# Kernel optimization log

Hardware: AMD Instinct MI355X
Metric: run time of the kernel (lower is better)

Reference implementation:

```python
import jax, jax.numpy as jnp
import numpy as np

GAMMA = 0.96875
ROPE_THETA = 10000.0


def _rope(x):
    # x: (B, S, d) -> rotary applied over interleaved pairs (torchtune-style)
    B, S, d = x.shape
    inv_freq = 1.0 / (ROPE_THETA ** (jnp.arange(0, d, 2, dtype=jnp.float32) / d))  # (d/2,)
    angles = jnp.arange(S, dtype=jnp.float32)[:, None] * inv_freq[None, :]  # (S, d/2)
    cos = jnp.cos(angles).astype(x.dtype)
    sin = jnp.sin(angles).astype(x.dtype)
    xs = x.reshape(B, S, d // 2, 2)
    x0, x1 = xs[..., 0], xs[..., 1]
    out = jnp.stack([x0 * cos - x1 * sin, x1 * cos + x0 * sin], axis=-1)
    return out.reshape(B, S, d)


def _decay_mask(S, dtype):
    n = jnp.arange(S)[:, None]
    m = jnp.arange(S)[None, :]
    diff = n - m
    # gamma^(n-m) for n>=m else 0; clamp exponent to avoid inf/nan
    D = jnp.exp(jnp.maximum(diff, 0).astype(jnp.float32) * np.log(GAMMA))
    return jnp.where(diff >= 0, D, 0.0).astype(dtype)


def setup_inputs() -> dict:
    key = jax.random.key(0)
    k1, k2, k3, k4 = jax.random.split(key, 4)
    H = 256
    X = jax.random.normal(k1, (4, 8192, H), dtype=jnp.float32)
    W_Q = jax.random.normal(k2, (H, H), dtype=jnp.float32) / H
    W_K = jax.random.normal(k3, (H, H), dtype=jnp.float32) / H
    W_V = jax.random.normal(k4, (H, H), dtype=jnp.float32) / H
    return {"X": X, "W_Q": W_Q, "W_K": W_K, "W_V": W_V}


def reference(X, W_Q, W_K, W_V):
    B, S, _ = X.shape
    D = _decay_mask(S, X.dtype)  # (S, S)
    Q = _rope(X @ W_Q)  # (B, S, d)
    K = _rope(X @ W_K)
    V = X @ W_V  # (B, S, v_dim)
    ret = jnp.einsum('bqd,bkd->bqk', Q, K) * D[None]  # (B, S, S)
    return ret @ V
```

## Files before the change

### kernel.cpp

```cpp
#include <hip/hip_runtime.h>
#include <hip/hip_bf16.h>

#define B_  4
#define S_  8192
#define H_  256
#define C_  128
#define NC_ 64
#define M_  (B_*S_)

typedef unsigned short u16;
typedef __attribute__((ext_vector_type(8))) short short8;
typedef __attribute__((ext_vector_type(4))) float f32x4;
typedef __attribute__((address_space(1))) void gas_t;
typedef __attribute__((address_space(3))) void las_t;

static constexpr float L2G   = -0.045803690f;
static constexpr float ROPE2 = -0.103810253f;

__device__ __forceinline__ u16 f2b(float x) {
  union { __hip_bfloat16 b; u16 u; } c; c.b = __float2bfloat16(x); return c.u;
}
__device__ __forceinline__ float b2f(u16 u) {
  union { u16 u; __hip_bfloat16 b; } c; c.u = u; return __bfloat162float(c.b);
}
__device__ __forceinline__ f32x4 mfma16(short8 a, short8 b, f32x4 c) {
  return __builtin_amdgcn_mfma_f32_16x16x32_bf16(a, b, c, 0, 0, 0);
}

__device__ __forceinline__ int sw4(int row) { return (row ^ (row >> 2)) & 3; }
__device__ __forceinline__ short8 fr32(const u16* base, int row, int slot) {
  return *reinterpret_cast<const short8*>(base + row*256 + (((slot&24)|((slot&7)^(row&7)))<<3));
}
__device__ __forceinline__ short8 fr16(const u16* base, int row, int slot) {
  return *reinterpret_cast<const short8*>(base + row*128 + (((slot&8)|((slot&7)^(row&7)))<<3));
}
__device__ __forceinline__ short8 fr4(const u16* base, int row, int slot) {
  return *reinterpret_cast<const short8*>(base + row*32 + ((slot ^ sw4(row))<<3));
}
__device__ __forceinline__ short8 fragr(const u16* lds, int row, int slot) {
  return *reinterpret_cast<const short8*>(lds + row*64 + ((slot ^ (row & 7)) << 3));
}

__device__ __forceinline__ void stageA(const u16* __restrict__ src, int stride,
                                       u16* smbase, int off, int t) {
  #pragma unroll
  for (int it = 0; it < 4; ++it) {
    const int u = it*256 + t, row = u >> 3, lsl = (u & 7) ^ (row & 7);
    const u16* gp = src + (size_t)row*stride + lsl*8;
    u16* lp = smbase + off + it*2048 + (t & 192)*8;
    __builtin_amdgcn_global_load_lds((gas_t*)gp, (las_t*)lp, 16, 0, 0);
  }
}
__device__ __forceinline__ void stageW(const u16* __restrict__ src, u16* dst, int t) {
  #pragma unroll
  for (int it = 0; it < 2; ++it) {
    const int u = it*512 + t, row = u >> 2, p = u & 3, s = p ^ sw4(row);
    const u16* gp = src + (size_t)row*256 + s*8;
    u16* lp = dst + (size_t)(it*512 + (t & ~63))*8;
    __builtin_amdgcn_global_load_lds((gas_t*)gp, (las_t*)lp, 16, 0, 0);
  }
}

__global__ __launch_bounds__(256) void prep(
    const float* __restrict__ Wq, const float* __restrict__ Wk,
    const float* __restrict__ Wv, u16* __restrict__ WhT, float* __restrict__ RTab)
{
  const int bid = blockIdx.x;
  if (bid < 96) {
    const int i = bid*256 + threadIdx.x;
    const int z = i >> 13, r = i & 8191;
    const int n = r >> 5, k0 = (r & 31) << 3;
    const float* W = (z == 0) ? Wq : (z == 1) ? Wk : Wv;
    u16 o[8];
    #pragma unroll
    for (int j = 0; j < 8; ++j) o[j] = f2b(W[(size_t)(k0 + j)*H_ + n]);
    *reinterpret_cast<uint4*>(WhT + ((size_t)z << 16) + n*H_ + k0) =
        *reinterpret_cast<uint4*>(o);
    return;
  }
  const int i = (bid - 96)*256 + threadIdx.x;
  const int s = i >> 7, h = i & 127;
  const float invf = exp2f(ROPE2 * (float)h);
  float sn, cs;
  sincosf((float)s * invf, &sn, &cs);
  *reinterpret_cast<float2*>(RTab + 2*((size_t)s*128 + h)) = make_float2(cs, sn);
}

__global__ __launch_bounds__(512, 2) void fused_chunk(
    const float* __restrict__ X, const u16* __restrict__ WhT,
    const float* __restrict__ RTab,
    u16* __restrict__ Qh, u16* __restrict__ Tt,
    u16* __restrict__ Scg, u16* __restrict__ VTg)
{
  __shared__ u16 SM[81920];
  u16* XS = SM;
  u16* WB = SM + 32768;
  u16* RB = SM + 49152;
  const int t = threadIdx.x, l = t & 63, wid = t >> 6;
  const int g = l >> 4, l15 = l & 15;
  const int mr = wid >> 2, nq = wid & 3;
  const int c = blockIdx.x, b = blockIdx.y;
  const float* Xc = X + ((size_t)(b*S_ + c*C_))*H_;
  const float4* RT4 = reinterpret_cast<const float4*>(RTab);

  stageW(WhT + 0, WB, t);
  #pragma unroll
  for (int it = 0; it < 8; ++it) {
    const int u = it*512 + t, row = u >> 5, sl = u & 31;
    const float* p = Xc + (size_t)row*256 + sl*8;
    float4 a = *reinterpret_cast<const float4*>(p);
    float4 bb = *reinterpret_cast<const float4*>(p + 4);
    u16 o[8] = {f2b(a.x), f2b(a.y), f2b(a.z), f2b(a.w),
                f2b(bb.x), f2b(bb.y), f2b(bb.z), f2b(bb.w)};
    *reinterpret_cast<uint4*>(XS + row*256 + (((sl&24)|((sl&7)^(row&7)))<<3)) =
        *reinterpret_cast<uint4*>(o);
  }
  __syncthreads();

  f32x4 qa[4][4] = {};
  for (int ks = 0; ks < 8; ++ks) {
    const u16* Wcur = WB + (ks&1)*8192;
    if (ks < 7) stageW(WhT + (ks+1)*32, WB + ((ks+1)&1)*8192, t);
    short8 a[4], bw[4];
    #pragma unroll
    for (int i = 0; i < 4; ++i) a[i] = fr32(XS, mr*64 + i*16 + l15, ks*4 + g);
    #pragma unroll
    for (int j = 0; j < 4; ++j) bw[j] = fr4(Wcur, nq*64 + j*16 + l15, g);
    #pragma unroll
    for (int i = 0; i < 4; ++i)
      #pragma unroll
      for (int j = 0; j < 4; ++j)
        qa[i][j] = mfma16(bw[j], a[i], qa[i][j]);
    __syncthreads();
  }
  #pragma unroll
  for (int i = 0; i < 4; ++i) {
    const int s = c*C_ + mr*64 + i*16 + l15;
    #pragma unroll
    for (int j = 0; j < 4; ++j) {
      const int n0 = nq*64 + j*16 + g*4;
      const float4 tb = RT4[(size_t)s*64 + (n0 >> 2)];
      const float x0 = qa[i][j][0], x1 = qa[i][j][1];
      const float x2 = qa[i][j][2], x3 = qa[i][j][3];
      qa[i][j][0] = x0*tb.x - x1*tb.y;  qa[i][j][1] = x1*tb.x + x0*tb.y;
      qa[i][j][2] = x2*tb.z - x3*tb.w;  qa[i][j][3] = x3*tb.z + x2*tb.w;
    }
  }
  #pragma unroll
  for (int i = 0; i < 4; ++i) {
    const int m = mr*64 + i*16 + l15;
    #pragma unroll
    for (int j = 0; j < 4; ++j) {
      const int n0 = nq*64 + j*16 + g*4;
      ushort4 pk;
      pk.x = f2b(qa[i][j][0]); pk.y = f2b(qa[i][j][1]);
      pk.z = f2b(qa[i][j][2]); pk.w = f2b(qa[i][j][3]);
      const int sl = n0 >> 3;
      *reinterpret_cast<ushort4*>(RB + m*256 + (((sl&24)|((sl&7)^(m&7)))<<3) + (n0&7)) = pk;
    }
  }
  __syncthreads();
  #pragma unroll
  for (int it = 0; it < 8; ++it) {
    const int u = it*512 + t, row = u >> 5, sl = u & 31;
    uint4 v = *reinterpret_cast<const uint4*>(RB + row*256 + (((sl&24)|((sl&7)^(row&7)))<<3));
    *reinterpret_cast<uint4*>(Qh + ((size_t)(b*S_ + c*C_ + row))*H_ + sl*8) = v;
  }

  f32x4 ka[4][4] = {};
  stageW(WhT + 65536, WB, t);
  __syncthreads();
  for (int ks = 0; ks < 8; ++ks) {
    const u16* Wcur = WB + (ks&1)*8192;
    if (ks < 7) stageW(WhT + 65536 + (ks+1)*32, WB + ((ks+1)&1)*8192, t);
    short8 a[4], bw[4];
    #pragma unroll
    for (int i = 0; i < 4; ++i) a[i] = fr32(XS, mr*64 + i*16 + l15, ks*4 + g);
    #pragma unroll
    for (int j = 0; j < 4; ++j) bw[j] = fr4(Wcur, nq*64 + j*16 + l15, g);
    #pragma unroll
    for (int i = 0; i < 4; ++i)
      #pragma unroll
      for (int j = 0; j < 4; ++j)
        ka[i][j] = mfma16(bw[j], a[i], ka[i][j]);
    __syncthreads();
  }
  #pragma unroll
  for (int i = 0; i < 4; ++i) {
    const int s = c*C_ + mr*64 + i*16 + l15;
    #pragma unroll
    for (int j = 0; j < 4; ++j) {
      const int n0 = nq*64 + j*16 + g*4;
      const float4 tb = RT4[(size_t)s*64 + (n0 >> 2)];
      const float x0 = ka[i][j][0], x1 = ka[i][j][1];
      const float x2 = ka[i][j][2], x3 = ka[i][j][3];
      ka[i][j][0] = x0*tb.x - x1*tb.y;  ka[i][j][1] = x1*tb.x + x0*tb.y;
      ka[i][j][2] = x2*tb.z - x3*tb.w;  ka[i][j][3] = x3*tb.z + x2*tb.w;
    }
  }

  const int smh = wid >> 2, sn0 = (wid & 3)*32;
  f32x4 sc[4][2] = {};
  #pragma unroll
  for (int h = 0; h < 2; ++h) {
    if (((wid >> 1) & 1) == h) {
      #pragma unroll
      for (int i = 0; i < 4; ++i) {
        const int m = mr*64 + i*16 + l15;
        #pragma unroll
        for (int j = 0; j < 4; ++j) {
          const int dl0 = (nq&1)*64 + j*16 + g*4;
          ushort4 pk;
          pk.x = f2b(ka[i][j][0]); pk.y = f2b(ka[i][j][1]);
          pk.z = f2b(ka[i][j][2]); pk.w = f2b(ka[i][j][3]);
          const int sl = dl0 >> 3;
          *reinterpret_cast<ushort4*>(WB + m*128 + (((sl&8)|((sl&7)^(m&7)))<<3) + (dl0&7)) = pk;
        }
      }
    }
    __syncthreads();
    #pragma unroll
    for (int kk = 0; kk < 4; ++kk) {
      short8 fa[4], fb[2];
      #pragma unroll
      for (int i = 0; i < 4; ++i) fa[i] = fr16(WB, smh*64 + i*16 + l15, kk*4 + g);
      #pragma unroll
      for (int j = 0; j < 2; ++j) fb[j] = fr32(RB, sn0 + j*16 + l15, h*16 + kk*4 + g);
      #pragma unroll
      for (int i = 0; i < 4; ++i)
        #pragma unroll
        for (int j = 0; j < 2; ++j)
          sc[i][j] = mfma16(fa[i], fb[j], sc[i][j]);
    }
    __syncthreads();
  }
  #pragma unroll
  for (int j = 0; j < 2; ++j) {
    const int n = sn0 + j*16 + l15;
    #pragma unroll
    for (int i = 0; i < 4; ++i) {
      const int m0 = smh*64 + i*16 + g*4;
      ushort4 pk;
      #pragma unroll
      for (int r = 0; r < 4; ++r) {
        const int m = m0 + r;
        const float sv = (n >= m) ? sc[i][j][r] * exp2f((float)(n - m)*L2G) : 0.f;
        reinterpret_cast<u16*>(&pk)[r] = f2b(sv);
      }
      const int sl = m0 >> 3;
      *reinterpret_cast<ushort4*>(WB + n*128 + (((sl&8)|((sl&7)^(n&7)))<<3) + (m0&7)) = pk;
    }
  }

  f32x4 va[4][4] = {};
  stageW(WhT + 2*65536, RB, t);
  __syncthreads();
  for (int ks = 0; ks < 8; ++ks) {
    const u16* Wcur = RB + (ks&1)*8192;
    if (ks < 7) stageW(WhT + 2*65536 + (ks+1)*32, RB + ((ks+1)&1)*8192, t);
    short8 a[4], bw[4];
    #pragma unroll
    for (int i = 0; i < 4; ++i) a[i] = fr32(XS, mr*64 + i*16 + l15, ks*4 + g);
    #pragma unroll
    for (int j = 0; j < 4; ++j) bw[j] = fr4(Wcur, nq*64 + j*16 + l15, g);
    #pragma unroll
    for (int i = 0; i < 4; ++i)
      #pragma unroll
      for (int j = 0; j < 4; ++j)
        va[i][j] = mfma16(a[i], bw[j], va[i][j]);
    __syncthreads();
  }

  {
    const size_t scb = ((size_t)(b*NC_ + c)) << 14;
    #pragma unroll
    for (int it = 0; it < 4; ++it) {
      const int u = it*512 + t, row = u >> 4, sl = u & 15;
      uint4 v = *reinterpret_cast<const uint4*>(WB + row*128 + (((sl&8)|((sl&7)^(row&7)))<<3));
      *reinterpret_cast<uint4*>(Scg + scb + (size_t)row*128 + sl*8) = v;
    }
  }

  #pragma unroll
  for (int jj = 0; jj < 4; ++jj) {
    const int j = nq*64 + jj*16 + l15;
    #pragma unroll
    for (int i = 0; i < 4; ++i) {
      const int m0 = mr*64 + i*16 + g*4;
      ushort4 pk;
      pk.x = f2b(va[i][jj][0]); pk.y = f2b(va[i][jj][1]);
      pk.z = f2b(va[i][jj][2]); pk.w = f2b(va[i][jj][3]);
      const int sl = m0 >> 3;
      *reinterpret_cast<ushort4*>(RB + j*128 + (((sl&8)|((sl&7)^(j&7)))<<3) + (m0&7)) = pk;
    }
  }
  #pragma unroll
  for (int i = 0; i < 4; ++i) {
    const int m = mr*64 + i*16 + l15;
    const float wd = exp2f((float)(C_ - 1 - m)*L2G);
    const int slm = m >> 3;
    #pragma unroll
    for (int jj = 0; jj < 4; ++jj) {
      #pragma unroll
      for (int r = 0; r < 4; ++r) {
        const int d = nq*64 + jj*16 + g*4 + r;
        XS[d*128 + (((slm&8)|((slm&7)^(d&7)))<<3) + (m&7)] = f2b(ka[i][jj][r] * wd);
      }
    }
  }
  __syncthreads();

  const int ih = wid & 1, jq = wid >> 1;
  {
    f32x4 tt[8][4] = {};
    #pragma unroll
    for (int kk = 0; kk < 4; ++kk) {
      short8 fk[8], fv[4];
      #pragma unroll
      for (int ii = 0; ii < 8; ++ii) fk[ii] = fr16(XS, ih*128 + ii*16 + l15, kk*4 + g);
      #pragma unroll
      for (int jj = 0; jj < 4; ++jj) fv[jj] = fr16(RB, jq*64 + jj*16 + l15, kk*4 + g);
      #pragma unroll
      for (int ii = 0; ii < 8; ++ii)
        #pragma unroll
        for (int jj = 0; jj < 4; ++jj)
          tt[ii][jj] = mfma16(fk[ii], fv[jj], tt[ii][jj]);
    }
    __syncthreads();

    {
      const size_t vtb = ((size_t)(b*NC_ + c)) << 15;
      #pragma unroll
      for (int it = 0; it < 8; ++it) {
        const int u = it*512 + t, row = u >> 4, sl = u & 15;
        uint4 v = *reinterpret_cast<const uint4*>(RB + row*128 + (((sl&8)|((sl&7)^(row&7)))<<3));
        *reinterpret_cast<uint4*>(VTg + vtb + (size_t)row*128 + sl*8) = v;
      }
    }

    const size_t tb = ((size_t)(b*NC_ + c)) << 16;
    #pragma unroll
    for (int p = 0; p < 2; ++p) {
      if ((jq >> 1) == p) {
        #pragma unroll
        for (int ii = 0; ii < 8; ++ii)
          #pragma unroll
          for (int jj = 0; jj < 4; ++jj) {
            const int jl = (jq&1)*64 + jj*16 + l15;
            const int i0 = ih*128 + ii*16 + g*4;
            ushort4 pk;
            pk.x = f2b(tt[ii][jj][0]); pk.y = f2b(tt[ii][jj][1]);
            pk.z = f2b(tt[ii][jj][2]); pk.w = f2b(tt[ii][jj][3]);
            const int sl = i0 >> 3;
            *reinterpret_cast<ushort4*>(XS + jl*256 + (((sl&24)|((sl&7)^(jl&7)))<<3) + (i0&7)) = pk;
          }
      }
      __syncthreads();
      #pragma unroll
      for (int it = 0; it < 8; ++it) {
        const int u = it*512 + t, row = u >> 5, sl = u & 31;
        uint4 v = *reinterpret_cast<const uint4*>(XS + row*256 + (((sl&24)|((sl&7)^(row&7)))<<3));
        *reinterpret_cast<uint4*>(Tt + tb + (size_t)(p*128 + row)*256 + sl*8) = v;
      }
      __syncthreads();
    }
  }
}

__global__ __launch_bounds__(256) void scan_state(u16* __restrict__ Tt)
{
  const unsigned e = blockIdx.x*256u + threadIdx.x;
  const unsigned b = e >> 15, el = (e & 32767u) << 1;
  const float gC = exp2f(128.0f * L2G);
  float r0 = 0.f, r1 = 0.f;
  const size_t base = (((size_t)b * NC_) << 16) + el;
  #pragma unroll
  for (int grp = 0; grp < 4; ++grp) {
    unsigned buf[16];
    #pragma unroll
    for (int i2 = 0; i2 < 16; ++i2)
      buf[i2] = *reinterpret_cast<const unsigned*>(Tt + base + (size_t)(grp*16 + i2)*65536);
    #pragma unroll
    for (int i2 = 0; i2 < 16; ++i2) {
      const unsigned v = buf[i2];
      *reinterpret_cast<unsigned*>(Tt + base + (size_t)(grp*16 + i2)*65536) =
          (unsigned)f2b(r0) | ((unsigned)f2b(r1) << 16);
      r0 = fmaf(gC, r0, b2f((u16)(v & 0xffff)));
      r1 = fmaf(gC, r1, b2f((u16)(v >> 16)));
    }
  }
}

__global__ __launch_bounds__(256) void out_kernel(
    const u16* __restrict__ Qh, const u16* __restrict__ Tt,
    const u16* __restrict__ Scg, const u16* __restrict__ VTg,
    float* __restrict__ Out)
{
  __shared__ u16 SM[32768];
  const int t = threadIdx.x, l = t & 63, wid = t >> 6;
  const int wr = wid >> 1, wc = wid & 1, g = l >> 4, l15 = l & 15;
  const int c = blockIdx.x, b = blockIdx.y, jh = blockIdx.z;
  const u16* Asrc = Qh + (size_t)(b*S_ + c*C_)*H_;
  const u16* Bsrc = Tt + (((size_t)(b*NC_ + c)) << 16) + (size_t)(jh*128)*H_;
  f32x4 acc[4][4] = {};

  stageA(Asrc, H_, SM, 0, t);
  stageA(Bsrc, H_, SM, 8192, t);
  __syncthreads();
  for (int ks = 0; ks < 4; ++ks) {
    const int cur = (ks & 1) * 16384;
    if (ks < 3) {
      stageA(Asrc + (ks+1)*64, H_, SM, 16384 - cur, t);
      stageA(Bsrc + (ks+1)*64, H_, SM, 16384 - cur + 8192, t);
    }
    #pragma unroll
    for (int kb = 0; kb < 2; ++kb) {
      short8 fq[4], ft[4];
      #pragma unroll
      for (int i = 0; i < 4; ++i) fq[i] = fragr(SM + cur, wr*64 + i*16 + l15, kb*4 + g);
      #pragma unroll
      for (int j = 0; j < 4; ++j) ft[j] = fragr(SM + cur + 8192, wc*64 + j*16 + l15, kb*4 + g);
      #pragma unroll
      for (int i = 0; i < 4; ++i)
        #pragma unroll
        for (int j = 0; j < 4; ++j)
          acc[i][j] = mfma16(ft[j], fq[i], acc[i][j]);
    }
    __syncthreads();
  }

  const u16* ScC = Scg + (((size_t)(b*NC_ + c)) << 14);
  const u16* VtC = VTg + (((size_t)(b*NC_ + c)) << 15) + (size_t)(jh*128)*128;
  stageA(ScC,      128, SM, 0,     t);
  stageA(VtC,      128, SM, 8192,  t);
  stageA(ScC + 64, 128, SM, 16384, t);
  stageA(VtC + 64, 128, SM, 24576, t);
  #pragma unroll
  for (int i = 0; i < 4; ++i) {
    const float gn = exp2f((float)(wr*64 + i*16 + l15 + 1) * L2G);
    #pragma unroll
    for (int j = 0; j < 4; ++j)
      #pragma unroll
      for (int r = 0; r < 4; ++r) acc[i][j][r] *= gn;
  }
  __syncthreads();

  #pragma unroll
  for (int ks2 = 0; ks2 < 2; ++ks2) {
    #pragma unroll
    for (int kb = 0; kb < 2; ++kb) {
      short8 fs[4], fv[4];
      #pragma unroll
      for (int i = 0; i < 4; ++i)
        fs[i] = fragr(SM + ks2*16384, wr*64 + i*16 + l15, kb*4 + g);
      #pragma unroll
      for (int j = 0; j < 4; ++j)
        fv[j] = fragr(SM + ks2*16384 + 8192, wc*64 + j*16 + l15, kb*4 + g);
      #pragma unroll
      for (int i = 0; i < 4; ++i)
        #pragma unroll
        for (int j = 0; j < 4; ++j)
          acc[i][j] = mfma16(fv[j], fs[i], acc[i][j]);
    }
  }
  __syncthreads();

  float* OL = reinterpret_cast<float*>(SM);
  for (int ph = 0; ph < 2; ++ph) {
    if (wr == ph) {
      #pragma unroll
      for (int i = 0; i < 4; ++i) {
        const int nl = i*16 + l15;
        #pragma unroll
        for (int j = 0; j < 4; ++j) {
          const int j0 = wc*64 + j*16 + g*4;
          const int sl = j0 >> 2;
          *reinterpret_cast<f32x4*>(OL + nl*128 + (((sl&24)|((sl&7)^(nl&7)))<<2)) = acc[i][j];
        }
      }
    }
    __syncthreads();
    #pragma unroll
    for (int it = 0; it < 8; ++it) {
      const int u = it*256 + t, nl = u >> 5, sl = u & 31;
      f32x4 v = *reinterpret_cast<const f32x4*>(OL + nl*128 + (((sl&24)|((sl&7)^(nl&7)))<<2));
      const size_t off = ((size_t)(b*S_ + c*C_ + ph*64 + nl))*256 + jh*128 + sl*4;
      *reinterpret_cast<f32x4*>(Out + off) = v;
    }
    __syncthreads();
  }
}

extern "C" void kernel_launch(void* const* d_in, const int* in_sizes, int n_in,
                              void* d_out, int out_size, void* d_ws, size_t ws_size,
                              hipStream_t stream) {
  const float* X  = (const float*)d_in[0];
  const float* Wq = (const float*)d_in[1];
  const float* Wk = (const float*)d_in[2];
  const float* Wv = (const float*)d_in[3];
  float* Out = (float*)d_out;
  u16* ws = (u16*)d_ws;
  u16*   WhT  = ws;
  float* RTab = (float*)(ws + 196608);
  u16*   Qh   = ws + 196608 + 4194304;
  u16*   Tt   = Qh + (size_t)M_*H_;
  u16*   Scg  = Tt + (size_t)B_*NC_*65536;
  u16*   VTg  = Scg + (size_t)B_*NC_*16384;

  prep<<<96 + 4096, 256, 0, stream>>>(Wq, Wk, Wv, WhT, RTab);
  fused_chunk<<<dim3(NC_, B_), 512, 0, stream>>>(X, WhT, RTab, Qh, Tt, Scg, VTg);
  scan_state<<<(B_*32768)/256, 256, 0, stream>>>(Tt);
  out_kernel<<<dim3(NC_, B_, 2), 256, 0, stream>>>(Qh, Tt, Scg, VTg, Out);
}
```

Baseline: 83.07 us.

## Fuse Q, K, V projection loops into one pass over X tile

Merges the three separate projection GEMM loops into a single k-loop that stages all three weight slices per step and reuses the same X fragments for Q, K and V MFMAs. This removes two extra rounds of X fragment LDS reads, two sets of barriers per k-step, and two pipeline prologues. The cost is three live accumulator arrays (48 f32x4 per thread) at once, which raises register pressure and risks spills at 512 threads with 2 blocks per CU. The shared-memory layout is reassigned into new regions to fit the larger weight staging buffer.

```diff
diff --git a/kernel.cpp b/kernel.cpp
--- a/kernel.cpp
+++ b/kernel.cpp
@@ -93,9 +93,13 @@
     u16* __restrict__ Scg, u16* __restrict__ VTg)
 {
   __shared__ u16 SM[81920];
-  u16* XS = SM;
-  u16* WB = SM + 32768;
-  u16* RB = SM + 49152;
+  u16* XS  = SM;
+  u16* WD  = SM + 32768;
+  u16* QRM = SM + 32768;
+  u16* KRM = SM + 65536;
+  u16* SCb = SM;
+  u16* KTW = SM + 16384;
+  u16* VTB = SM + 49152;
   const int t = threadIdx.x, l = t & 63, wid = t >> 6;
   const int g = l >> 4, l15 = l & 15;
   const int mr = wid >> 2, nq = wid & 3;
@@ -103,7 +107,9 @@
   const float* Xc = X + ((size_t)(b*S_ + c*C_))*H_;
   const float4* RT4 = reinterpret_cast<const float4*>(RTab);
 
-  stageW(WhT + 0, WB, t);
+  stageW(WhT + 0,       WD + 0,     t);
+  stageW(WhT + 65536,   WD + 8192,  t);
+  stageW(WhT + 2*65536, WD + 16384, t);
   #pragma unroll
   for (int it = 0; it < 8; ++it) {
     const int u = it*512 + t, row = u >> 5, sl = u & 31;
@@ -117,22 +123,42 @@
   }
   __syncthreads();
 
-  f32x4 qa[4][4] = {};
+  f32x4 qa[4][4] = {}, ka[4][4] = {}, va[4][4] = {};
   for (int ks = 0; ks < 8; ++ks) {
-    const u16* Wcur = WB + (ks&1)*8192;
-    if (ks < 7) stageW(WhT + (ks+1)*32, WB + ((ks+1)&1)*8192, t);
+    const u16* Wb = WD + (ks&1)*24576;
+    if (ks < 7) {
+      u16* Wn = WD + ((ks+1)&1)*24576;
+      stageW(WhT + (ks+1)*32,           Wn,         t);
+      stageW(WhT + 65536 + (ks+1)*32,   Wn + 8192,  t);
+      stageW(WhT + 2*65536 + (ks+1)*32, Wn + 16384, t);
+    }
     short8 a[4], bw[4];
     #pragma unroll
     for (int i = 0; i < 4; ++i) a[i] = fr32(XS, mr*64 + i*16 + l15, ks*4 + g);
     #pragma unroll
-    for (int j = 0; j < 4; ++j) bw[j] = fr4(Wcur, nq*64 + j*16 + l15, g);
+    for (int j = 0; j < 4; ++j) bw[j] = fr4(Wb, nq*64 + j*16 + l15, g);
     #pragma unroll
     for (int i = 0; i < 4; ++i)
       #pragma unroll
       for (int j = 0; j < 4; ++j)
         qa[i][j] = mfma16(bw[j], a[i], qa[i][j]);
-    __syncthreads();
-  }
+    #pragma unroll
+    for (int j = 0; j < 4; ++j) bw[j] = fr4(Wb + 8192, nq*64 + j*16 + l15, g);
+    #pragma unroll
+    for (int i = 0; i < 4; ++i)
+      #pragma unroll
+      for (int j = 0; j < 4; ++j)
+        ka[i][j] = mfma16(bw[j], a[i], ka[i][j]);
+    #pragma unroll
+    for (int j = 0; j < 4; ++j) bw[j] = fr4(Wb + 16384, nq*64 + j*16 + l15, g);
+    #pragma unroll
+    for (int i = 0; i < 4; ++i)
+      #pragma unroll
+      for (int j = 0; j < 4; ++j)
+        va[i][j] = mfma16(a[i], bw[j], va[i][j]);
+    __syncthreads();
+  }
+
   #pragma unroll
   for (int i = 0; i < 4; ++i) {
     const int s = c*C_ + mr*64 + i*16 + l15;
@@ -140,10 +166,12 @@
     for (int j = 0; j < 4; ++j) {
       const int n0 = nq*64 + j*16 + g*4;
       const float4 tb = RT4[(size_t)s*64 + (n0 >> 2)];
-      const float x0 = qa[i][j][0], x1 = qa[i][j][1];
-      const float x2 = qa[i][j][2], x3 = qa[i][j][3];
+      float x0 = qa[i][j][0], x1 = qa[i][j][1], x2 = qa[i][j][2], x3 = qa[i][j][3];
       qa[i][j][0] = x0*tb.x - x1*tb.y;  qa[i][j][1] = x1*tb.x + x0*tb.y;
       qa[i][j][2] = x2*tb.z - x3*tb.w;  qa[i][j][3] = x3*tb.z + x2*tb.w;
+      x0 = ka[i][j][0]; x1 = ka[i][j][1]; x2 = ka[i][j][2]; x3 = ka[i][j][3];
+      ka[i][j][0] = x0*tb.x - x1*tb.y;  ka[i][j][1] = x1*tb.x + x0*tb.y;
+      ka[i][j][2] = x2*tb.z - x3*tb.w;  ka[i][j][3] = x3*tb.z + x2*tb.w;
     }
   }
   #pragma unroll
@@ -156,47 +184,15 @@
       pk.x = f2b(qa[i][j][0]); pk.y = f2b(qa[i][j][1]);
       pk.z = f2b(qa[i][j][2]); pk.w = f2b(qa[i][j][3]);
       const int sl = n0 >> 3;
-      *reinterpret_cast<ushort4*>(RB + m*256 + (((sl&24)|((sl&7)^(m&7)))<<3) + (n0&7)) = pk;
+      *reinterpret_cast<ushort4*>(QRM + m*256 + (((sl&24)|((sl&7)^(m&7)))<<3) + (n0&7)) = pk;
     }
   }
   __syncthreads();
   #pragma unroll
   for (int it = 0; it < 8; ++it) {
     const int u = it*512 + t, row = u >> 5, sl = u & 31;
-    uint4 v = *reinterpret_cast<const uint4*>(RB + row*256 + (((sl&24)|((sl&7)^(row&7)))<<3));
+    uint4 v = *reinterpret_cast<const uint4*>(QRM + row*256 + (((sl&24)|((sl&7)^(row&7)))<<3));
     *reinterpret_cast<uint4*>(Qh + ((size_t)(b*S_ + c*C_ + row))*H_ + sl*8) = v;
-  }
-
-  f32x4 ka[4][4] = {};
-  stageW(WhT + 65536, WB, t);
-  __syncthreads();
-  for (int ks = 0; ks < 8; ++ks) {
-    const u16* Wcur = WB + (ks&1)*8192;
-    if (ks < 7) stageW(WhT + 65536 + (ks+1)*32, WB + ((ks+1)&1)*8192, t);
-    short8 a[4], bw[4];
-    #pragma unroll
-    for (int i = 0; i < 4; ++i) a[i] = fr32(XS, mr*64 + i*16 + l15, ks*4 + g);
-    #pragma unroll
-    for (int j = 0; j < 4; ++j) bw[j] = fr4(Wcur, nq*64 + j*16 + l15, g);
-    #pragma unroll
-    for (int i = 0; i < 4; ++i)
-      #pragma unroll
-      for (int j = 0; j < 4; ++j)
-        ka[i][j] = mfma16(bw[j], a[i], ka[i][j]);
-    __syncthreads();
-  }
-  #pragma unroll
-  for (int i = 0; i < 4; ++i) {
-    const int s = c*C_ + mr*64 + i*16 + l15;
-    #pragma unroll
-    for (int j = 0; j < 4; ++j) {
-      const int n0 = nq*64 + j*16 + g*4;
-      const float4 tb = RT4[(size_t)s*64 + (n0 >> 2)];
-      const float x0 = ka[i][j][0], x1 = ka[i][j][1];
-      const float x2 = ka[i][j][2], x3 = ka[i][j][3];
-      ka[i][j][0] = x0*tb.x - x1*tb.y;  ka[i][j][1] = x1*tb.x + x0*tb.y;
-      ka[i][j][2] = x2*tb.z - x3*tb.w;  ka[i][j][3] = x3*tb.z + x2*tb.w;
-    }
   }
 
   const int smh = wid >> 2, sn0 = (wid & 3)*32;
@@ -214,7 +210,7 @@
           pk.x = f2b(ka[i][j][0]); pk.y = f2b(ka[i][j][1]);
           pk.z = f2b(ka[i][j][2]); pk.w = f2b(ka[i][j][3]);
           const int sl = dl0 >> 3;
-          *reinterpret_cast<ushort4*>(WB + m*128 + (((sl&8)|((sl&7)^(m&7)))<<3) + (dl0&7)) = pk;
+          *reinterpret_cast<ushort4*>(KRM + m*128 + (((sl&8)|((sl&7)^(m&7)))<<3) + (dl0&7)) = pk;
         }
       }
     }
@@ -223,9 +219,9 @@
     for (int kk = 0; kk < 4; ++kk) {
       short8 fa[4], fb[2];
       #pragma unroll
-      for (int i = 0; i < 4; ++i) fa[i] = fr16(WB, smh*64 + i*16 + l15, kk*4 + g);
-      #pragma unroll
-      for (int j = 0; j < 2; ++j) fb[j] = fr32(RB, sn0 + j*16 + l15, h*16 + kk*4 + g);
+      for (int i = 0; i < 4; ++i) fa[i] = fr16(KRM, smh*64 + i*16 + l15, kk*4 + g);
+      #pragma unroll
+      for (int j = 0; j < 2; ++j) fb[j] = fr32(QRM, sn0 + j*16 + l15, h*16 + kk*4 + g);
       #pragma unroll
       for (int i = 0; i < 4; ++i)
         #pragma unroll
@@ -248,35 +244,17 @@
         reinterpret_cast<u16*>(&pk)[r] = f2b(sv);
       }
       const int sl = m0 >> 3;
-      *reinterpret_cast<ushort4*>(WB + n*128 + (((sl&8)|((sl&7)^(n&7)))<<3) + (m0&7)) = pk;
-    }
-  }
-
-  f32x4 va[4][4] = {};
-  stageW(WhT + 2*65536, RB, t);
-  __syncthreads();
-  for (int ks = 0; ks < 8; ++ks) {
-    const u16* Wcur = RB + (ks&1)*8192;
-    if (ks < 7) stageW(WhT + 2*65536 + (ks+1)*32, RB + ((ks+1)&1)*8192, t);
-    short8 a[4], bw[4];
-    #pragma unroll
-    for (int i = 0; i < 4; ++i) a[i] = fr32(XS, mr*64 + i*16 + l15, ks*4 + g);
-    #pragma unroll
-    for (int j = 0; j < 4; ++j) bw[j] = fr4(Wcur, nq*64 + j*16 + l15, g);
-    #pragma unroll
-    for (int i = 0; i < 4; ++i)
-      #pragma unroll
-      for (int j = 0; j < 4; ++j)
-        va[i][j] = mfma16(a[i], bw[j], va[i][j]);
-    __syncthreads();
-  }
+      *reinterpret_cast<ushort4*>(SCb + n*128 + (((sl&8)|((sl&7)^(n&7)))<<3) + (m0&7)) = pk;
+    }
+  }
+  __syncthreads();
 
   {
     const size_t scb = ((size_t)(b*NC_ + c)) << 14;
     #pragma unroll
     for (int it = 0; it < 4; ++it) {
       const int u = it*512 + t, row = u >> 4, sl = u & 15;
-      uint4 v = *reinterpret_cast<const uint4*>(WB + row*128 + (((sl&8)|((sl&7)^(row&7)))<<3));
+      uint4 v = *reinterpret_cast<const uint4*>(SCb + row*128 + (((sl&8)|((sl&7)^(row&7)))<<3));
       *reinterpret_cast<uint4*>(Scg + scb + (size_t)row*128 + sl*8) = v;
     }
   }
@@ -291,7 +269,7 @@
       pk.x = f2b(va[i][jj][0]); pk.y = f2b(va[i][jj][1]);
       pk.z = f2b(va[i][jj][2]); pk.w = f2b(va[i][jj][3]);
       const int sl = m0 >> 3;
-      *reinterpret_cast<ushort4*>(RB + j*128 + (((sl&8)|((sl&7)^(j&7)))<<3) + (m0&7)) = pk;
+      *reinterpret_cast<ushort4*>(VTB + j*128 + (((sl&8)|((sl&7)^(j&7)))<<3) + (m0&7)) = pk;
     }
   }
   #pragma unroll
@@ -304,7 +282,7 @@
       #pragma unroll
       for (int r = 0; r < 4; ++r) {
         const int d = nq*64 + jj*16 + g*4 + r;
-        XS[d*128 + (((slm&8)|((slm&7)^(d&7)))<<3) + (m&7)] = f2b(ka[i][jj][r] * wd);
+        KTW[d*128 + (((slm&8)|((slm&7)^(d&7)))<<3) + (m&7)] = f2b(ka[i][jj][r] * wd);
       }
     }
   }
@@ -317,9 +295,9 @@
     for (int kk = 0; kk < 4; ++kk) {
       short8 fk[8], fv[4];
       #pragma unroll
-      for (int ii = 0; ii < 8; ++ii) fk[ii] = fr16(XS, ih*128 + ii*16 + l15, kk*4 + g);
-      #pragma unroll
-      for (int jj = 0; jj < 4; ++jj) fv[jj] = fr16(RB, jq*64 + jj*16 + l15, kk*4 + g);
+      for (int ii = 0; ii < 8; ++ii) fk[ii] = fr16(KTW, ih*128 + ii*16 + l15, kk*4 + g);
+      #pragma unroll
+      for (int jj = 0; jj < 4; ++jj) fv[jj] = fr16(VTB, jq*64 + jj*16 + l15, kk*4 + g);
       #pragma unroll
       for (int ii = 0; ii < 8; ++ii)
         #pragma unroll
@@ -333,7 +311,7 @@
       #pragma unroll
       for (int it = 0; it < 8; ++it) {
         const int u = it*512 + t, row = u >> 4, sl = u & 15;
-        uint4 v = *reinterpret_cast<const uint4*>(RB + row*128 + (((sl&8)|((sl&7)^(row&7)))<<3));
+        uint4 v = *reinterpret_cast<const uint4*>(VTB + row*128 + (((sl&8)|((sl&7)^(row&7)))<<3));
         *reinterpret_cast<uint4*>(VTg + vtb + (size_t)row*128 + sl*8) = v;
       }
     }
@@ -352,14 +330,14 @@
             pk.x = f2b(tt[ii][jj][0]); pk.y = f2b(tt[ii][jj][1]);
             pk.z = f2b(tt[ii][jj][2]); pk.w = f2b(tt[ii][jj][3]);
             const int sl = i0 >> 3;
-            *reinterpret_cast<ushort4*>(XS + jl*256 + (((sl&24)|((sl&7)^(jl&7)))<<3) + (i0&7)) = pk;
+            *reinterpret_cast<ushort4*>(SM + jl*256 + (((sl&24)|((sl&7)^(jl&7)))<<3) + (i0&7)) = pk;
           }
       }
       __syncthreads();
       #pragma unroll
       for (int it = 0; it < 8; ++it) {
         const int u = it*512 + t, row = u >> 5, sl = u & 31;
-        uint4 v = *reinterpret_cast<const uint4*>(XS + row*256 + (((sl&24)|((sl&7)^(row&7)))<<3));
+        uint4 v = *reinterpret_cast<const uint4*>(SM + row*256 + (((sl&24)|((sl&7)^(row&7)))<<3));
         *reinterpret_cast<uint4*>(Tt + tb + (size_t)(p*128 + row)*256 + sl*8) = v;
       }
       __syncthreads();
```

Measured after the change: 127.5 us. 53.5% more time.
